# Kernel tuning notes

Measured on AMD Instinct MI355X. Metric: run time of the kernel, lower is better.

Reference implementation:

```python
import jax, jax.numpy as jnp
import numpy as np

B, NP, FIN = 128, 64, 2048   # graphs, nodes per graph, input feat
H, D = 8, 64                 # GAT heads, per-head dim
HD = H * D                   # 512
HID = 1024                   # Set2Set channels (concat of two 512 convs)
R2 = 16.0                    # radius^2 (r=4)
SLOPE = 0.2                  # GATConv leaky_relu slope
EPS = 0.1                    # BatchNorm eps


def setup_inputs() -> dict:
    key = jax.random.key(0)
    ks = jax.random.split(key, 20)
    s = 0.02
    inp = {}
    inp['x'] = jax.random.normal(ks[0], (B * NP, FIN), jnp.float32)
    inp['pos'] = jax.random.uniform(ks[1], (B * NP, 2), jnp.float32) * 20.0
    inp['batch'] = jnp.repeat(jnp.arange(B, dtype=jnp.int32), NP)
    # lin01: Linear(2048,2048,bias=False) + BN(2048, eps=0.1) (eval mode)
    inp['W0'] = jax.random.normal(ks[2], (FIN, 2048), jnp.float32) * s
    inp['bn0_g'] = jnp.ones((2048,), jnp.float32)
    inp['bn0_b'] = jnp.zeros((2048,), jnp.float32)
    inp['bn0_m'] = jnp.zeros((2048,), jnp.float32)
    inp['bn0_v'] = jnp.ones((2048,), jnp.float32)
    # two GATConv(2048, 64, heads=8)
    inp['Wg1'] = jax.random.normal(ks[3], (2048, HD), jnp.float32) * s
    inp['as1'] = jax.random.normal(ks[4], (H, D), jnp.float32) * s
    inp['ad1'] = jax.random.normal(ks[5], (H, D), jnp.float32) * s
    inp['b1'] = jnp.zeros((HD,), jnp.float32)
    inp['Wg2'] = jax.random.normal(ks[6], (2048, HD), jnp.float32) * s
    inp['as2'] = jax.random.normal(ks[7], (H, D), jnp.float32) * s
    inp['ad2'] = jax.random.normal(ks[8], (H, D), jnp.float32) * s
    inp['b2'] = jnp.zeros((HD,), jnp.float32)
    # Set2Set LSTM: 2 layers, input 2*HID, hidden HID
    inp['Wih0'] = jax.random.normal(ks[9], (4 * HID, 2 * HID), jnp.float32) * s
    inp['Whh0'] = jax.random.normal(ks[10], (4 * HID, HID), jnp.float32) * s
    inp['bih0'] = jnp.zeros((4 * HID,), jnp.float32)
    inp['bhh0'] = jnp.zeros((4 * HID,), jnp.float32)
    inp['Wih1'] = jax.random.normal(ks[11], (4 * HID, HID), jnp.float32) * s
    inp['Whh1'] = jax.random.normal(ks[12], (4 * HID, HID), jnp.float32) * s
    inp['bih1'] = jnp.zeros((4 * HID,), jnp.float32)
    inp['bhh1'] = jnp.zeros((4 * HID,), jnp.float32)
    # lin2: Linear(2048,1024,bias=False) + BN(1024, eps=0.1)
    inp['W2'] = jax.random.normal(ks[13], (2 * HID, HID), jnp.float32) * s
    inp['bn2_g'] = jnp.ones((HID,), jnp.float32)
    inp['bn2_b'] = jnp.zeros((HID,), jnp.float32)
    inp['bn2_m'] = jnp.zeros((HID,), jnp.float32)
    inp['bn2_v'] = jnp.ones((HID,), jnp.float32)
    # lin3: Linear(1024, 10)
    inp['W3'] = jax.random.normal(ks[14], (HID, 10), jnp.float32) * s
    inp['b3'] = jnp.zeros((10,), jnp.float32)
    return inp


def _bn(x, g, b, m, v):
    return (x - m) * jax.lax.rsqrt(v + EPS) * g + b


def _gat(xb, adj, Wg, a_src, a_dst, bias):
    # xb: [B, NP, 2048], adj: [B, NP, NP] bool (diag True = self-loops)
    h = (xb @ Wg).reshape(B, NP, H, D)
    es = jnp.einsum('bnhd,hd->bnh', h, a_src)   # source-node score
    ed = jnp.einsum('bnhd,hd->bnh', h, a_dst)   # target-node score
    # e[b, i, j, h]: edge j -> i
    e = jax.nn.leaky_relu(ed[:, :, None, :] + es[:, None, :, :], SLOPE)
    e = jnp.where(adj[..., None], e, -jnp.inf)
    alpha = jax.nn.softmax(e, axis=2)           # softmax over neighbors j
    out = jnp.einsum('bijh,bjhd->bihd', alpha, h).reshape(B, NP, HD)
    return out + bias


def _cell(inp, h, c, Wih, Whh, bih, bhh):
    z = inp @ Wih.T + h @ Whh.T + bih + bhh
    i, f, g, o = jnp.split(z, 4, axis=-1)
    c = jax.nn.sigmoid(f) * c + jax.nn.sigmoid(i) * jnp.tanh(g)
    return jax.nn.sigmoid(o) * jnp.tanh(c), c


def _forward(x, pos, W0, bn0_g, bn0_b, bn0_m, bn0_v,
             Wg1, as1, ad1, b1, Wg2, as2, ad2, b2,
             Wih0, Whh0, bih0, bhh0, Wih1, Whh1, bih1, bhh1,
             W2, bn2_g, bn2_b, bn2_m, bn2_v, W3, b3):
    # radius_graph(r=4) per graph; GATConv re-adds self-loops -> diag True
    p = pos.reshape(B, NP, 2)
    d2 = jnp.sum((p[:, :, None, :] - p[:, None, :, :]) ** 2, axis=-1)
    adj = d2 <= R2
    x = _bn(jax.nn.relu(x @ W0), bn0_g, bn0_b, bn0_m, bn0_v)  # dropout: eval
    xb = x.reshape(B, NP, 2048)
    g1 = jax.nn.relu(_gat(xb, adj, Wg1, as1, ad1, b1))
    g2 = jax.nn.relu(_gat(xb, adj, Wg2, as2, ad2, b2))
    x2 = jnp.concatenate([g1, g2], axis=-1)                   # [B, NP, 1024]
    # Set2Set: processing_steps=2, 2-layer LSTM
    q_star = jnp.zeros((B, 2 * HID), x2.dtype)
    h0 = c0 = h1 = c1 = jnp.zeros((B, HID), x2.dtype)
    for _ in range(2):
        h0, c0 = _cell(q_star, h0, c0, Wih0, Whh0, bih0, bhh0)
        h1, c1 = _cell(h0, h1, c1, Wih1, Whh1, bih1, bhh1)
        e = jnp.einsum('bnd,bd->bn', x2, h1)
        a = jax.nn.softmax(e, axis=1)                         # per-graph softmax
        r = jnp.einsum('bn,bnd->bd', a, x2)
        q_star = jnp.concatenate([h1, r], axis=-1)            # [B, 2048]
    y = _bn(jax.nn.relu(q_star @ W2), bn2_g, bn2_b, bn2_m, bn2_v)
    return y @ W3 + b3                                        # [B, 10] ('A2')


def reference(x, pos, batch, W0, bn0_g, bn0_b, bn0_m, bn0_v,
              Wg1, as1, ad1, b1, Wg2, as2, ad2, b2,
              Wih0, Whh0, bih0, bhh0, Wih1, Whh1, bih1, bhh1,
              W2, bn2_g, bn2_b, bn2_m, bn2_v, W3, b3):
    # batch ids are implicit in the fixed [B, NP] layout
    return _forward(x, pos, W0, bn0_g, bn0_b, bn0_m, bn0_v,
                    Wg1, as1, ad1, b1, Wg2, as2, ad2, b2,
                    Wih0, Whh0, bih0, bhh0, Wih1, Whh1, bih1, bhh1,
                    W2, bn2_g, bn2_b, bn2_m, bn2_v, W3, b3)
```

## Files before the change

kernel.cpp:

```cpp
#include <hip/hip_runtime.h>
#include <hip/hip_bf16.h>

typedef unsigned short u16;
typedef __attribute__((ext_vector_type(8))) short short8;
typedef __attribute__((ext_vector_type(4))) float f32x4;
typedef unsigned long long u64;

#define DI __device__ __forceinline__

DI u16 f2b(float f){
  unsigned u = __float_as_uint(f);
  unsigned r = 0x7fffu + ((u >> 16) & 1u);
  return (u16)((u + r) >> 16);
}
DI float b2f(u16 u){ return __uint_as_float((unsigned)u << 16); }

DI void gl_lds16(const void* g, void* l){
  __builtin_amdgcn_global_load_lds((const __attribute__((address_space(1))) void*)g,
                                   (__attribute__((address_space(3))) void*)l, 16, 0, 0);
}

constexpr size_t O_XBF = 0;
constexpr size_t O_W0T = O_XBF + 33554432;
constexpr size_t O_WGT = O_W0T + 8388608;
constexpr size_t O_W2T = O_WGT + 4194304;
constexpr size_t O_XB  = O_W2T + 4194304;
constexpr size_t O_H   = O_XB  + 33554432;
constexpr size_t O_ES  = O_H   + 33554432;
constexpr size_t O_ED  = O_ES  + 524288;
constexpr size_t O_ADJ = O_ED  + 524288;
constexpr size_t O_SC0 = O_ADJ + 65536;
constexpr size_t O_SH0 = O_SC0 + 8192;
constexpr size_t O_SC2 = O_SH0 + 8192;
constexpr size_t O_SH2 = O_SC2 + 4096;
constexpr size_t O_LB0 = O_SH2 + 4096;
constexpr size_t O_LB1 = O_LB0 + 16384;
constexpr size_t S_AC0 = 0;
constexpr size_t S_AC1 = S_AC0 + 786432;
constexpr size_t S_C0  = S_AC1 + 524288;
constexpr size_t S_C1  = S_C0  + 524288;
constexpr size_t S_H1F = S_C1  + 524288;
constexpr size_t S_ZP  = S_H1F + 524288;
constexpr size_t S_E   = S_ZP  + 16777216;
constexpr size_t S_Z1U = S_E   + 32768;

__global__ __launch_bounds__(256) void setup_all(
    const float* __restrict__ x,
    const float* __restrict__ W0, const float* __restrict__ Wg1,
    const float* __restrict__ Wg2, const float* __restrict__ W2,
    const float* __restrict__ g0, const float* __restrict__ b0, const float* __restrict__ m0, const float* __restrict__ v0,
    const float* __restrict__ g2, const float* __restrict__ b2, const float* __restrict__ m2, const float* __restrict__ v2,
    const float* __restrict__ bih0, const float* __restrict__ bhh0,
    const float* __restrict__ bih1, const float* __restrict__ bhh1,
    const float* __restrict__ pos,
    u16* __restrict__ xbf, u16* __restrict__ w0t, u16* __restrict__ wgt, u16* __restrict__ w2t,
    float* __restrict__ sc0, float* __restrict__ sh0, float* __restrict__ sc2, float* __restrict__ sh2,
    float* __restrict__ lb0, float* __restrict__ lb1, u64* __restrict__ adjm)
{
  __shared__ float tile[32][33];
  __shared__ float px[4][64], py[4][64];
  int bx = blockIdx.x, t = threadIdx.x;
  if(bx < 8192){
    int idx = bx * 256 + t;
    int r = idx >> 8, c8 = (idx & 255) << 3;
    const float* src = x + (size_t)r * 2048 + c8;
    float4 v0 = *(const float4*)src;
    float4 v1 = *(const float4*)(src + 4);
    short8 ov;
    ov[0] = (short)f2b(v0.x); ov[1] = (short)f2b(v0.y); ov[2] = (short)f2b(v0.z); ov[3] = (short)f2b(v0.w);
    ov[4] = (short)f2b(v1.x); ov[5] = (short)f2b(v1.y); ov[6] = (short)f2b(v1.z); ov[7] = (short)f2b(v1.w);
    *(short8*)(xbf + (size_t)r * 2048 + c8) = ov;
  } else if(bx < 16384){
    int bx2 = bx - 8192;
    int cx = bx2 & 127, by = bx2 >> 7;
    const float* src; u16* dst; int C, droff;
    if(cx < 64){      src = W0;  dst = w0t; C = 2048; droff = 0; }
    else if(cx < 80){ src = Wg1; dst = wgt; C = 512;  droff = 0;   cx -= 64; }
    else if(cx < 96){ src = Wg2; dst = wgt; C = 512;  droff = 512; cx -= 80; }
    else {            src = W2;  dst = w2t; C = 1024; droff = 0;   cx -= 96; }
    int c0 = cx * 32, r0 = by * 32;
    int tx = t & 31, ty = t >> 5;
    for(int i = 0; i < 4; i++)
      tile[ty + 8*i][tx] = src[(size_t)(r0 + ty + 8*i) * C + c0 + tx];
    __syncthreads();
    for(int i = 0; i < 4; i++)
      dst[(size_t)(droff + c0 + ty + 8*i) * 2048 + r0 + tx] = f2b(tile[tx][ty + 8*i]);
  } else if(bx < 16400){
    int tt = (bx - 16384) * 256 + t;
    if(tt < 2048){ float s = g0[tt] * rsqrtf(v0[tt] + 0.1f); sc0[tt] = s; sh0[tt] = b0[tt] - m0[tt] * s; }
    if(tt < 1024){ float s = g2[tt] * rsqrtf(v2[tt] + 0.1f); sc2[tt] = s; sh2[tt] = b2[tt] - m2[tt] * s; }
    lb0[tt] = bih0[tt] + bhh0[tt];
    lb1[tt] = bih1[tt] + bhh1[tt];
  } else {
    int w = t >> 6, l = t & 63;
    int g = (bx - 16400) * 4 + w;
    float2 p = ((const float2*)pos)[g * 64 + l];
    px[w][l] = p.x; py[w][l] = p.y;
    __syncthreads();
    float xi = p.x, yi = p.y;
    u64 m = 0;
    for(int j = 0; j < 64; j++){
      float dx = xi - px[w][j], dy = yi - py[w][j];
      if(dx * dx + dy * dy <= 16.0f) m |= (1ull << j);
    }
    adjm[g * 64 + l] = m;
  }
}

template<int MODE>
__global__ __launch_bounds__(256) void gemm_bf16(
    const u16* __restrict__ A, const u16* __restrict__ Bt,
    float* __restrict__ Cf, u16* __restrict__ Cb,
    const float* __restrict__ p1, const float* __restrict__ p2,
    int M, int N, int K)
{
  constexpr int BM = 128, BN = 128, BK = 64;
  __shared__ alignas(16) u16 Al[BM * BK];
  __shared__ alignas(16) u16 Bl[BN * BK];
  int m0 = blockIdx.x * BM, n0 = blockIdx.y * BN;
  int t = threadIdx.x, w = t >> 6, l = t & 63;
  int wm = (w >> 1) * 64, wn = (w & 1) * 64;
  f32x4 acc[4][4];
  for(int a = 0; a < 4; a++) for(int b = 0; b < 4; b++) acc[a][b] = {0.f, 0.f, 0.f, 0.f};

  const short8* Ap = (const short8*)Al;
  const short8* Bp = (const short8*)Bl;

  for(int k0 = 0; k0 < K; k0 += BK){
    #pragma unroll
    for(int u = t; u < BM * 8; u += 256){
      int r = u >> 3, c = u & 7;
      gl_lds16(A + (size_t)(m0 + r) * K + k0 + ((c ^ (r & 7)) << 3), Al + u * 8);
    }
    #pragma unroll
    for(int u = t; u < BN * 8; u += 256){
      int r = u >> 3, c = u & 7;
      gl_lds16(Bt + (size_t)(n0 + r) * K + k0 + ((c ^ (r & 7)) << 3), Bl + u * 8);
    }
    __syncthreads();
    #pragma unroll
    for(int ks = 0; ks < 2; ks++){
      int kc = ks * 4 + (l >> 4);
      short8 av[4], bv[4];
      #pragma unroll
      for(int mi = 0; mi < 4; mi++){ int r = wm + mi * 16 + (l & 15); av[mi] = Ap[r * 8 + (kc ^ (r & 7))]; }
      #pragma unroll
      for(int ni = 0; ni < 4; ni++){ int r = wn + ni * 16 + (l & 15); bv[ni] = Bp[r * 8 + (kc ^ (r & 7))]; }
      #pragma unroll
      for(int mi = 0; mi < 4; mi++)
        #pragma unroll
        for(int ni = 0; ni < 4; ni++)
          acc[mi][ni] = __builtin_amdgcn_mfma_f32_16x16x32_bf16(av[mi], bv[ni], acc[mi][ni], 0, 0, 0);
    }
    __syncthreads();
  }

  int cr = m0 + wm + ((l >> 4) << 2);
  int cc = n0 + wn + (l & 15);
  for(int mi = 0; mi < 4; mi++)
    for(int ni = 0; ni < 4; ni++)
      for(int r = 0; r < 4; r++){
        int row = cr + mi * 16 + r, col = cc + ni * 16;
        float v = acc[mi][ni][r];
        if(MODE == 1){ v = fmaxf(v, 0.f) * p1[col] + p2[col]; Cb[(size_t)row * N + col] = f2b(v); }
        else if(MODE == 3){ Cb[(size_t)row * N + col] = f2b(v); }
        else { Cf[(size_t)row * N + col] = v; }
      }
}

__global__ __launch_bounds__(256) void gemm_sk(
    const u16* __restrict__ A, const u16* __restrict__ Bt, float* __restrict__ Cf,
    int N, int lda, int ldb, int kPer)
{
  constexpr int BM = 128, BN = 64, BK = 64;
  __shared__ alignas(16) u16 Al[BM * BK];
  __shared__ alignas(16) u16 Bl[BN * BK];
  int n0 = blockIdx.x * BN;
  int kb = blockIdx.y * kPer;
  float* C = Cf + (size_t)blockIdx.y * 128 * N;
  int t = threadIdx.x, w = t >> 6, l = t & 63;
  int wm = (w >> 1) * 64, wn = (w & 1) * 32;
  f32x4 acc[4][2];
  for(int a = 0; a < 4; a++) for(int b = 0; b < 2; b++) acc[a][b] = {0.f, 0.f, 0.f, 0.f};

  const short8* Ap = (const short8*)Al;
  const short8* Bp = (const short8*)Bl;

  for(int k0 = kb; k0 < kb + kPer; k0 += BK){
    #pragma unroll
    for(int u = t; u < BM * 8; u += 256){
      int r = u >> 3, c = u & 7;
      gl_lds16(A + (size_t)r * lda + k0 + ((c ^ (r & 7)) << 3), Al + u * 8);
    }
    #pragma unroll
    for(int u = t; u < BN * 8; u += 256){
      int r = u >> 3, c = u & 7;
      gl_lds16(Bt + (size_t)(n0 + r) * ldb + k0 + ((c ^ (r & 7)) << 3), Bl + u * 8);
    }
    __syncthreads();
    #pragma unroll
    for(int ks = 0; ks < 2; ks++){
      int kc = ks * 4 + (l >> 4);
      short8 av[4], bv[2];
      #pragma unroll
      for(int mi = 0; mi < 4; mi++){ int r = wm + mi * 16 + (l & 15); av[mi] = Ap[r * 8 + (kc ^ (r & 7))]; }
      #pragma unroll
      for(int ni = 0; ni < 2; ni++){ int r = wn + ni * 16 + (l & 15); bv[ni] = Bp[r * 8 + (kc ^ (r & 7))]; }
      #pragma unroll
      for(int mi = 0; mi < 4; mi++)
        #pragma unroll
        for(int ni = 0; ni < 2; ni++)
          acc[mi][ni] = __builtin_amdgcn_mfma_f32_16x16x32_bf16(av[mi], bv[ni], acc[mi][ni], 0, 0, 0);
    }
    __syncthreads();
  }

  int cr = wm + ((l >> 4) << 2);
  int cc = n0 + wn + (l & 15);
  for(int mi = 0; mi < 4; mi++)
    for(int ni = 0; ni < 2; ni++)
      for(int r = 0; r < 4; r++)
        C[(size_t)(cr + mi * 16 + r) * N + cc + ni * 16] = acc[mi][ni][r];
}

__global__ __launch_bounds__(256) void gemm_skf(
    const u16* __restrict__ A, const float* __restrict__ Wih, const float* __restrict__ Whh,
    float* __restrict__ Cf, int N, int lda, int Kih, int Khh, int kPer)
{
  constexpr int BM = 128, BN = 64, BK = 64;
  __shared__ alignas(16) u16 Al[BM * BK];
  __shared__ alignas(16) u16 Bl[BN * BK];
  int n0 = blockIdx.x * BN;
  int kb = blockIdx.y * kPer;
  float* C = Cf + (size_t)blockIdx.y * 128 * N;
  int t = threadIdx.x, w = t >> 6, l = t & 63;
  int wm = (w >> 1) * 64, wn = (w & 1) * 32;
  f32x4 acc[4][2];
  for(int a = 0; a < 4; a++) for(int b = 0; b < 2; b++) acc[a][b] = {0.f, 0.f, 0.f, 0.f};

  const short8* Ap = (const short8*)Al;
  const short8* Bp = (const short8*)Bl;

  for(int k0 = kb; k0 < kb + kPer; k0 += BK){
    #pragma unroll
    for(int u = t; u < BM * 8; u += 256){
      int r = u >> 3, c = u & 7;
      gl_lds16(A + (size_t)r * lda + k0 + ((c ^ (r & 7)) << 3), Al + u * 8);
    }
    #pragma unroll
    for(int u = t; u < BN * 8; u += 256){
      int r = u >> 3, c = u & 7;
      int gk = k0 + c * 8;
      const float* src = (gk < Kih) ? (Wih + (size_t)(n0 + r) * Kih + gk)
                                    : (Whh + (size_t)(n0 + r) * Khh + (gk - Kih));
      float4 v0 = *(const float4*)src;
      float4 v1 = *(const float4*)(src + 4);
      short8 ov;
      ov[0] = (short)f2b(v0.x); ov[1] = (short)f2b(v0.y); ov[2] = (short)f2b(v0.z); ov[3] = (short)f2b(v0.w);
      ov[4] = (short)f2b(v1.x); ov[5] = (short)f2b(v1.y); ov[6] = (short)f2b(v1.z); ov[7] = (short)f2b(v1.w);
      ((short8*)Bl)[r * 8 + (c ^ (r & 7))] = ov;
    }
    __syncthreads();
    #pragma unroll
    for(int ks = 0; ks < 2; ks++){
      int kc = ks * 4 + (l >> 4);
      short8 av[4], bv[2];
      #pragma unroll
      for(int mi = 0; mi < 4; mi++){ int r = wm + mi * 16 + (l & 15); av[mi] = Ap[r * 8 + (kc ^ (r & 7))]; }
      #pragma unroll
      for(int ni = 0; ni < 2; ni++){ int r = wn + ni * 16 + (l & 15); bv[ni] = Bp[r * 8 + (kc ^ (r & 7))]; }
      #pragma unroll
      for(int mi = 0; mi < 4; mi++)
        #pragma unroll
        for(int ni = 0; ni < 2; ni++)
          acc[mi][ni] = __builtin_amdgcn_mfma_f32_16x16x32_bf16(av[mi], bv[ni], acc[mi][ni], 0, 0, 0);
    }
    __syncthreads();
  }

  int cr = wm + ((l >> 4) << 2);
  int cc = n0 + wn + (l & 15);
  for(int mi = 0; mi < 4; mi++)
    for(int ni = 0; ni < 2; ni++)
      for(int r = 0; r < 4; r++)
        C[(size_t)(cr + mi * 16 + r) * N + cc + ni * 16] = acc[mi][ni][r];
}

__global__ __launch_bounds__(256) void gat_attn2(const u64* __restrict__ adjm,
    const u16* __restrict__ h,
    const float* __restrict__ as1, const float* __restrict__ ad1,
    const float* __restrict__ as2, const float* __restrict__ ad2,
    const float* __restrict__ b1, const float* __restrict__ b2,
    u16* __restrict__ x2b){
  int b = blockIdx.x;
  int cv = blockIdx.y >> 3, hh = blockIdx.y & 7;
  __shared__ float hst[64][64];
  __shared__ float alphaL[64][65];
  __shared__ float esl[64], edl[64];
  __shared__ u64 adjs[64];
  int t = threadIdx.x, w = t >> 6, l = t & 63;
  {
    int j = t >> 2, d0 = (t & 3) * 16;
    const u16* hr = h + (size_t)(b * 64 + j) * 1024 + cv * 512 + hh * 64 + d0;
    #pragma unroll
    for(int k = 0; k < 16; k++) hst[j][d0 + k] = b2f(hr[k]);
  }
  if(t < 64) adjs[t] = adjm[b * 64 + t];
  __syncthreads();
  float aSl = ((cv ? as2 : as1) + hh * 64)[l];
  float aDl = ((cv ? ad2 : ad1) + hh * 64)[l];
  for(int it = 0; it < 16; it++){
    int j = it * 4 + w;
    float v = hst[j][l];
    float ps = v * aSl, pd = v * aDl;
    for(int o = 32; o; o >>= 1){ ps += __shfl_xor(ps, o); pd += __shfl_xor(pd, o); }
    if(l == 0){ esl[j] = ps; edl[j] = pd; }
  }
  __syncthreads();
  for(int it = 0; it < 16; it++){
    int i = it * 4 + w;
    bool on = (adjs[i] >> l) & 1;
    float e = edl[i] + esl[l];
    e = e > 0.f ? e : 0.2f * e;
    float mx = on ? e : -1e30f;
    for(int o = 32; o; o >>= 1) mx = fmaxf(mx, __shfl_xor(mx, o));
    float p = on ? __expf(e - mx) : 0.f;
    float s = p;
    for(int o = 32; o; o >>= 1) s += __shfl_xor(s, o);
    alphaL[i][l] = p / s;
  }
  __syncthreads();
  int i = t >> 2, q = t & 3;
  float acc[16];
  #pragma unroll
  for(int k = 0; k < 16; k++) acc[k] = 0.f;
  for(int j = 0; j < 64; j++){
    float al = alphaL[i][j];
    const float* hr = &hst[j][q * 16];
    #pragma unroll
    for(int k = 0; k < 16; k++) acc[k] += al * hr[k];
  }
  const float* bias = (cv ? b2 : b1) + hh * 64 + q * 16;
  u16* op = x2b + (size_t)(b * 64 + i) * 1024 + cv * 512 + hh * 64 + q * 16;
  #pragma unroll
  for(int k = 0; k < 16; k++) op[k] = f2b(fmaxf(acc[k] + bias[k], 0.f));
}

__global__ __launch_bounds__(256) void s2s0_gemv(const float* __restrict__ Wih1,
    const float* __restrict__ lb1, const float* __restrict__ lb0, float* __restrict__ z1u){
  __shared__ float hs[1024];
  int t = threadIdx.x;
  for(int i = t; i < 1024; i += 256){
    float zi = lb0[i], zg = lb0[2048 + i], zo = lb0[3072 + i];
    float cn = (1.f / (1.f + __expf(-zi))) * tanhf(zg);
    hs[i] = (1.f / (1.f + __expf(-zo))) * tanhf(cn);
  }
  __syncthreads();
  int w = t >> 6, l = t & 63;
  int r = blockIdx.x * 4 + w;
  const float* wr = Wih1 + (size_t)r * 1024;
  float s = 0.f;
  #pragma unroll
  for(int k = 0; k < 16; k++) s += wr[l + 64 * k] * hs[l + 64 * k];
  for(int o = 32; o; o >>= 1) s += __shfl_xor(s, o);
  if(l == 0) z1u[r] = s + lb1[r];
}

__global__ void lstm_gate0(const float* __restrict__ zp, const float* __restrict__ lb,
                           float* __restrict__ c, u16* __restrict__ ac0, u16* __restrict__ ac1,
                           int ns){
  int t = blockIdx.x * 256 + threadIdx.x;
  int b = t >> 10, j = t & 1023;
  size_t base = (size_t)b * 4096;
  float zi = 0, zf = 0, zg = 0, zo = 0;
  for(int s = 0; s < ns; s++){
    const float* zr = zp + (size_t)s * 524288 + base;
    zi += zr[j]; zf += zr[1024 + j]; zg += zr[2048 + j]; zo += zr[3072 + j];
  }
  zi += lb[j]; zf += lb[1024 + j]; zg += lb[2048 + j]; zo += lb[3072 + j];
  float ci = c[t];
  float si = 1.f / (1.f + __expf(-zi)), sf = 1.f / (1.f + __expf(-zf)), so = 1.f / (1.f + __expf(-zo));
  float cn = sf * ci + si * tanhf(zg);
  c[t] = cn;
  u16 hb = f2b(so * tanhf(cn));
  ac0[(size_t)b * 3072 + 2048 + j] = hb;
  ac1[(size_t)b * 2048 + j] = hb;
}

__global__ void lstm_gate1(const float* __restrict__ zp, const float* __restrict__ lb,
                           float* __restrict__ c, float* __restrict__ h1f,
                           u16* __restrict__ ac1, u16* __restrict__ ac0, int ns){
  int t = blockIdx.x * 256 + threadIdx.x;
  int b = t >> 10, j = t & 1023;
  size_t base = (size_t)b * 4096;
  float zi = 0, zf = 0, zg = 0, zo = 0;
  for(int s = 0; s < ns; s++){
    const float* zr = zp + (size_t)s * 524288 + base;
    zi += zr[j]; zf += zr[1024 + j]; zg += zr[2048 + j]; zo += zr[3072 + j];
  }
  zi += lb[j]; zf += lb[1024 + j]; zg += lb[2048 + j]; zo += lb[3072 + j];
  float ci = c[t];
  float si = 1.f / (1.f + __expf(-zi)), sf = 1.f / (1.f + __expf(-zf)), so = 1.f / (1.f + __expf(-zo));
  float cn = sf * ci + si * tanhf(zg);
  c[t] = cn;
  float hn = so * tanhf(cn);
  h1f[t] = hn;
  u16 hb = f2b(hn);
  ac1[(size_t)b * 2048 + 1024 + j] = hb;
  ac0[(size_t)b * 3072 + j] = hb;
}

template<int STEP>
__global__ __launch_bounds__(256) void s2s_e(const u16* __restrict__ x2b,
    const float* __restrict__ h1, const float* __restrict__ z1u, float* __restrict__ e){
  __shared__ float h1s[1024];
  int t = threadIdx.x, w = t >> 6, l = t & 63;
  int node = blockIdx.x * 4 + w;
  int b = node >> 6;
  for(int i = t; i < 1024; i += 256){
    if(STEP == 0){
      float zi = z1u[i], zg = z1u[2048 + i], zo = z1u[3072 + i];
      float cn = (1.f / (1.f + __expf(-zi))) * tanhf(zg);
      h1s[i] = (1.f / (1.f + __expf(-zo))) * tanhf(cn);
    } else {
      h1s[i] = h1[(size_t)b * 1024 + i];
    }
  }
  __syncthreads();
  const u16* xr = x2b + (size_t)node * 1024;
  float s = 0.f;
  #pragma unroll
  for(int k = 0; k < 16; k++){
    int d = k * 64 + l;
    s += b2f(xr[d]) * h1s[d];
  }
  for(int o = 32; o; o >>= 1) s += __shfl_xor(s, o);
  if(l == 0) e[node] = s;
}

template<int STEP>
__global__ __launch_bounds__(256) void s2s_r(const u16* __restrict__ x2b,
    const float* __restrict__ e, u16* __restrict__ ac0,
    const float* __restrict__ lb0, const float* __restrict__ z1u,
    u16* __restrict__ ac1, float* __restrict__ c0b, float* __restrict__ c1b){
  int b = blockIdx.x, sl = blockIdx.y;
  __shared__ float al[64];
  int t = threadIdx.x;
  if(t < 64){
    float v = e[b * 64 + t];
    float mx = v;
    for(int o = 32; o; o >>= 1) mx = fmaxf(mx, __shfl_xor(mx, o));
    float p = __expf(v - mx);
    float ss = p;
    for(int o = 32; o; o >>= 1) ss += __shfl_xor(ss, o);
    al[t] = p / ss;
  }
  __syncthreads();
  int d = sl * 256 + t;
  const u16* xp = x2b + (size_t)b * 65536 + d;
  float r = 0.f;
  #pragma unroll 8
  for(int j = 0; j < 64; j++) r += al[j] * b2f(xp[j * 1024]);
  ac0[(size_t)b * 3072 + 1024 + d] = f2b(r);
  if(STEP == 0){
    float zi0 = lb0[d], zg0 = lb0[2048 + d], zo0 = lb0[3072 + d];
    float c0 = (1.f / (1.f + __expf(-zi0))) * tanhf(zg0);
    float h0 = (1.f / (1.f + __expf(-zo0))) * tanhf(c0);
    float zi1 = z1u[d], zg1 = z1u[2048 + d], zo1 = z1u[3072 + d];
    float c1 = (1.f / (1.f + __expf(-zi1))) * tanhf(zg1);
    float h1 = (1.f / (1.f + __expf(-zo1))) * tanhf(c1);
    c0b[(size_t)b * 1024 + d] = c0;
    c1b[(size_t)b * 1024 + d] = c1;
    u16 h0b = f2b(h0), h1b = f2b(h1);
    ac0[(size_t)b * 3072 + d] = h1b;
    ac0[(size_t)b * 3072 + 2048 + d] = h0b;
    ac1[(size_t)b * 2048 + d] = h0b;
    ac1[(size_t)b * 2048 + 1024 + d] = h1b;
  }
}

__global__ __launch_bounds__(256) void lin3(const float* __restrict__ zp2,
    const float* __restrict__ sc2, const float* __restrict__ sh2,
    const float* __restrict__ W3, const float* __restrict__ b3, float* __restrict__ out){
  int b = blockIdx.x;
  __shared__ float yl[1024];
  int t = threadIdx.x, w = t >> 6, l = t & 63;
  for(int d = t; d < 1024; d += 256){
    float v = 0.f;
    for(int s = 0; s < 8; s++) v += zp2[(size_t)s * 131072 + b * 1024 + d];
    yl[d] = fmaxf(v, 0.f) * sc2[d] + sh2[d];
  }
  __syncthreads();
  for(int n = w; n < 10; n += 4){
    float s = 0.f;
    for(int d = l; d < 1024; d += 64) s += yl[d] * W3[d * 10 + n];
    for(int o = 32; o; o >>= 1) s += __shfl_xor(s, o);
    if(l == 0) out[b * 10 + n] = s + b3[n];
  }
}

extern "C" void kernel_launch(void* const* d_in, const int* in_sizes, int n_in,
                              void* d_out, int out_size, void* d_ws, size_t ws_size,
                              hipStream_t stream){
  const float* x    = (const float*)d_in[0];
  const float* pos  = (const float*)d_in[1];
  const float* W0   = (const float*)d_in[3];
  const float* bn0g = (const float*)d_in[4];
  const float* bn0b = (const float*)d_in[5];
  const float* bn0m = (const float*)d_in[6];
  const float* bn0v = (const float*)d_in[7];
  const float* Wg1  = (const float*)d_in[8];
  const float* as1  = (const float*)d_in[9];
  const float* ad1  = (const float*)d_in[10];
  const float* b1   = (const float*)d_in[11];
  const float* Wg2  = (const float*)d_in[12];
  const float* as2  = (const float*)d_in[13];
  const float* ad2  = (const float*)d_in[14];
  const float* b2   = (const float*)d_in[15];
  const float* Wih0 = (const float*)d_in[16];
  const float* Whh0 = (const float*)d_in[17];
  const float* bih0 = (const float*)d_in[18];
  const float* bhh0 = (const float*)d_in[19];
  const float* Wih1 = (const float*)d_in[20];
  const float* Whh1 = (const float*)d_in[21];
  const float* bih1 = (const float*)d_in[22];
  const float* bhh1 = (const float*)d_in[23];
  const float* W2   = (const float*)d_in[24];
  const float* bn2g = (const float*)d_in[25];
  const float* bn2b = (const float*)d_in[26];
  const float* bn2m = (const float*)d_in[27];
  const float* bn2v = (const float*)d_in[28];
  const float* W3   = (const float*)d_in[29];
  const float* b3   = (const float*)d_in[30];

  char* ws = (char*)d_ws;
  u16*   xbf  = (u16*)(ws + O_XBF);
  u16*   x2b  = (u16*)(ws + O_XBF);
  u16*   w0t  = (u16*)(ws + O_W0T);
  u16*   wgt  = (u16*)(ws + O_WGT);
  u16*   w2t  = (u16*)(ws + O_W2T);
  u16*   xb   = (u16*)(ws + O_XB);
  u16*   hb   = (u16*)(ws + O_H);
  u64*   adjm = (u64*)(ws + O_ADJ);
  float* sc0  = (float*)(ws + O_SC0);
  float* sh0  = (float*)(ws + O_SH0);
  float* sc2  = (float*)(ws + O_SC2);
  float* sh2  = (float*)(ws + O_SH2);
  float* lb0  = (float*)(ws + O_LB0);
  float* lb1  = (float*)(ws + O_LB1);
  char*  s2sb = ws + O_H;
  u16*   ac0  = (u16*)(s2sb + S_AC0);
  u16*   ac1  = (u16*)(s2sb + S_AC1);
  float* c0b  = (float*)(s2sb + S_C0);
  float* c1b  = (float*)(s2sb + S_C1);
  float* h1f  = (float*)(s2sb + S_H1F);
  float* zp   = (float*)(s2sb + S_ZP);
  float* ebuf = (float*)(s2sb + S_E);
  float* z1u  = (float*)(s2sb + S_Z1U);

  setup_all<<<16432, 256, 0, stream>>>(x, W0, Wg1, Wg2, W2,
                                       bn0g, bn0b, bn0m, bn0v, bn2g, bn2b, bn2m, bn2v,
                                       bih0, bhh0, bih1, bhh1, pos,
                                       xbf, w0t, wgt, w2t, sc0, sh0, sc2, sh2, lb0, lb1, adjm);

  gemm_bf16<1><<<dim3(64, 16), 256, 0, stream>>>(xbf, w0t, nullptr, xb, sc0, sh0, 8192, 2048, 2048);
  gemm_bf16<3><<<dim3(64, 8), 256, 0, stream>>>(xb, wgt, nullptr, hb, nullptr, nullptr, 8192, 1024, 2048);
  gat_attn2<<<dim3(128, 16), 256, 0, stream>>>(adjm, hb, as1, ad1, as2, ad2, b1, b2, x2b);

  s2s0_gemv<<<1024, 256, 0, stream>>>(Wih1, lb1, lb0, z1u);
  s2s_e<0><<<2048, 256, 0, stream>>>(x2b, nullptr, z1u, ebuf);
  s2s_r<0><<<dim3(128, 4), 256, 0, stream>>>(x2b, ebuf, ac0, lb0, z1u, ac1, c0b, c1b);

  gemm_skf<<<dim3(64, 8), 256, 0, stream>>>(ac0, Wih0, Whh0, zp, 4096, 3072, 2048, 1024, 384);
  lstm_gate0<<<512, 256, 0, stream>>>(zp, lb0, c0b, ac0, ac1, 8);
  gemm_skf<<<dim3(64, 8), 256, 0, stream>>>(ac1, Wih1, Whh1, zp, 4096, 2048, 1024, 1024, 256);
  lstm_gate1<<<512, 256, 0, stream>>>(zp, lb1, c1b, h1f, ac1, ac0, 8);
  s2s_e<1><<<2048, 256, 0, stream>>>(x2b, h1f, nullptr, ebuf);
  s2s_r<1><<<dim3(128, 4), 256, 0, stream>>>(x2b, ebuf, ac0, nullptr, nullptr, nullptr, nullptr, nullptr);

  gemm_sk<<<dim3(16, 8), 256, 0, stream>>>(ac0, w2t, zp, 1024, 3072, 2048, 256);
  lin3<<<128, 256, 0, stream>>>(zp, sc2, sh2, W3, b3, (float*)d_out);
}
```

Baseline: 303.2 us.

## Replace first GEMM with 256x256-tile 8-wave pipelined kernel using direct LDS loads

Adds a new GEMM kernel for the lin01 layer (8192x2048x2048) that uses 256x256 block tiles, 512 threads and double-buffered LDS filled by global_load_lds. The K-loop is split into phases, so loads for later tiles overlap MFMA compute, with partial vmcnt waits and barriers between phases. XOR swizzling avoids LDS bank conflicts. The larger tile is meant to raise operand reuse and hide memory latency. It uses more LDS and registers per block and gives fewer blocks (256) to spread across CUs.

```diff
diff --git a/kernel.cpp b/kernel.cpp
--- a/kernel.cpp
+++ b/kernel.cpp
@@ -107,6 +107,126 @@
   }
 }
 
+#define STAGE_A(buf, half, kt)                                                        \
+  { _Pragma("unroll")                                                                 \
+    for(int ld = 0; ld < 2; ld++){                                                    \
+      int u = ld * 512 + t;                                                           \
+      int r = (u >> 3) + (half) * 128, c = u & 7;                                     \
+      gl_lds16(A + (size_t)(m0 + r) * K + (kt) * 64 + ((c ^ (r & 7)) << 3),           \
+               LA + (buf) * 16384 + ((half) * 1024 + u) * 8);                         \
+    } }
+#define STAGE_B(buf, half, kt)                                                        \
+  { _Pragma("unroll")                                                                 \
+    for(int ld = 0; ld < 2; ld++){                                                    \
+      int u = ld * 512 + t;                                                           \
+      int r = (u >> 3) + (half) * 128, c = u & 7;                                     \
+      gl_lds16(Bt + (size_t)(n0 + r) * K + (kt) * 64 + ((c ^ (r & 7)) << 3),          \
+               LB + (buf) * 16384 + ((half) * 1024 + u) * 8);                         \
+    } }
+#define COMPUTE(buf, q)                                                               \
+  { if((q) == 0){                                                                     \
+      _Pragma("unroll")                                                               \
+      for(int nb = 0; nb < 4; nb++)                                                   \
+        _Pragma("unroll")                                                             \
+        for(int k2 = 0; k2 < 2; k2++){                                                \
+          int col = wn + nb * 16 + (l & 15);                                          \
+          int kc = k2 * 4 + (l >> 4);                                                 \
+          bfr[nb][k2] = Bp[(buf) * 2048 + col * 8 + (kc ^ (col & 7))];                \
+        }                                                                             \
+    }                                                                                 \
+    short8 af[2][2];                                                                  \
+    _Pragma("unroll")                                                                 \
+    for(int rb = 0; rb < 2; rb++)                                                     \
+      _Pragma("unroll")                                                               \
+      for(int k2 = 0; k2 < 2; k2++){                                                  \
+        int row = wm + (q) * 32 + rb * 16 + (l & 15);                                 \
+        int kc = k2 * 4 + (l >> 4);                                                   \
+        af[rb][k2] = Ap[(buf) * 2048 + row * 8 + (kc ^ (row & 7))];                   \
+      }                                                                               \
+    _Pragma("unroll")                                                                 \
+    for(int rb = 0; rb < 2; rb++)                                                     \
+      _Pragma("unroll")                                                               \
+      for(int nb = 0; nb < 4; nb++)                                                   \
+        _Pragma("unroll")                                                             \
+        for(int k2 = 0; k2 < 2; k2++)                                                 \
+          acc[(q) * 2 + rb][nb] = __builtin_amdgcn_mfma_f32_16x16x32_bf16(            \
+              af[rb][k2], bfr[nb][k2], acc[(q) * 2 + rb][nb], 0, 0, 0);               \
+  }
+#define PHASE_BAR() { __builtin_amdgcn_s_barrier(); __builtin_amdgcn_sched_barrier(0); }
+#define VM4() { asm volatile("s_waitcnt vmcnt(4)" ::: "memory"); __builtin_amdgcn_sched_barrier(0); }
+
+__global__ __launch_bounds__(512, 2) void gemm8p(
+    const u16* __restrict__ A, const u16* __restrict__ Bt, u16* __restrict__ Cb,
+    const float* __restrict__ p1, const float* __restrict__ p2,
+    int M, int N, int K)
+{
+  __shared__ alignas(16) u16 LA[2 * 16384];
+  __shared__ alignas(16) u16 LB[2 * 16384];
+  int m0 = blockIdx.x * 256, n0 = blockIdx.y * 256;
+  int t = threadIdx.x, w = t >> 6, l = t & 63;
+  int wm = (w >> 2) * 128, wn = (w & 3) * 64;
+  int nt = K >> 6, ni = nt >> 1;
+  f32x4 acc[8][4];
+  #pragma unroll
+  for(int a = 0; a < 8; a++)
+    #pragma unroll
+    for(int b = 0; b < 4; b++) acc[a][b] = {0.f, 0.f, 0.f, 0.f};
+  short8 bfr[4][2];
+  const short8* Ap = (const short8*)LA;
+  const short8* Bp = (const short8*)LB;
+
+  STAGE_A(0, 0, 0); STAGE_A(0, 1, 0); STAGE_B(0, 0, 0); STAGE_B(0, 1, 0);
+  STAGE_B(1, 0, 1); STAGE_B(1, 1, 1);
+  VM4();
+  PHASE_BAR();
+
+  for(int i = 0; i < ni; i++){
+    int t1 = 2 * i + 1;
+    int t2 = (2 * i + 2 < nt) ? 2 * i + 2 : nt - 1;
+    int t3 = (2 * i + 3 < nt) ? 2 * i + 3 : nt - 1;
+    STAGE_A(1, 0, t1); STAGE_A(1, 1, t1);
+    COMPUTE(0, 0);
+    PHASE_BAR();
+    STAGE_B(0, 0, t2);
+    COMPUTE(0, 1);
+    PHASE_BAR();
+    STAGE_B(0, 1, t2);
+    COMPUTE(0, 2);
+    PHASE_BAR();
+    COMPUTE(0, 3);
+    VM4();
+    PHASE_BAR();
+    STAGE_A(0, 0, t2);
+    COMPUTE(1, 0);
+    PHASE_BAR();
+    STAGE_A(0, 1, t2);
+    COMPUTE(1, 1);
+    PHASE_BAR();
+    STAGE_B(1, 0, t3);
+    COMPUTE(1, 2);
+    PHASE_BAR();
+    STAGE_B(1, 1, t3);
+    COMPUTE(1, 3);
+    VM4();
+    PHASE_BAR();
+  }
+  asm volatile("s_waitcnt vmcnt(0)" ::: "memory");
+
+  int cc = n0 + wn + (l & 15);
+  int r4 = (l >> 4) << 2;
+  #pragma unroll
+  for(int ar = 0; ar < 8; ar++)
+    #pragma unroll
+    for(int nb = 0; nb < 4; nb++)
+      #pragma unroll
+      for(int r = 0; r < 4; r++){
+        int row = m0 + wm + ar * 16 + r4 + r, col = cc + nb * 16;
+        float v = acc[ar][nb][r];
+        v = fmaxf(v, 0.f) * p1[col] + p2[col];
+        Cb[(size_t)row * N + col] = f2b(v);
+      }
+}
+
 template<int MODE>
 __global__ __launch_bounds__(256) void gemm_bf16(
     const u16* __restrict__ A, const u16* __restrict__ Bt,
@@ -563,7 +683,7 @@
                                        bih0, bhh0, bih1, bhh1, pos,
                                        xbf, w0t, wgt, w2t, sc0, sh0, sc2, sh2, lb0, lb1, adjm);
 
-  gemm_bf16<1><<<dim3(64, 16), 256, 0, stream>>>(xbf, w0t, nullptr, xb, sc0, sh0, 8192, 2048, 2048);
+  gemm8p<<<dim3(32, 8), 512, 0, stream>>>(xbf, w0t, xb, sc0, sh0, 8192, 2048, 2048);
   gemm_bf16<3><<<dim3(64, 8), 256, 0, stream>>>(xb, wgt, nullptr, hb, nullptr, nullptr, 8192, 1024, 2048);
   gat_attn2<<<dim3(128, 16), 256, 0, stream>>>(adjm, hb, as1, ad1, as2, ad2, b1, b2, x2b);
 
```

New measurement: 283.6 us. 1.07x faster.
